# Kernel optimization log

Measured on AMD Instinct MI355X. Metric: run time of the kernel, lower is better.

The kernel has to match this reference:

```python
import jax, jax.numpy as jnp
import numpy as np

RC = 64   # residual_channels
SC = 64   # skip_channels
LAYERS = 10
STACKS = 3
N_LAYERS = LAYERS * STACKS


def _conv1x1(w, b, x):
    # w: [O, I, 1], b: [O], x: [B, I, T] -> [B, O, T]
    return jnp.einsum('oi,bit->bot', w[:, :, 0], x) + b[None, :, None]


def setup_inputs() -> dict:
    key = jax.random.key(0)
    ks = jax.random.split(key, 16)
    s = 0.05  # small init keeps 30-layer residual stack numerically tame
    B, T = 4, 32768
    inp = {
        'x': jax.random.normal(ks[0], (B, 1, T), dtype=jnp.float32),
        'start_w': jax.random.normal(ks[1], (RC, 1, 1), jnp.float32) * s,
        'start_b': jax.random.normal(ks[2], (RC,), jnp.float32) * s,
        'dil_w': jax.random.normal(ks[3], (N_LAYERS, 2 * RC, RC, 2), jnp.float32) * s,
        'dil_b': jax.random.normal(ks[4], (N_LAYERS, 2 * RC), jnp.float32) * s,
        'res_w': jax.random.normal(ks[5], (N_LAYERS, RC, RC, 1), jnp.float32) * s,
        'res_b': jax.random.normal(ks[6], (N_LAYERS, RC), jnp.float32) * s,
        'skip_w': jax.random.normal(ks[7], (N_LAYERS, SC, RC, 1), jnp.float32) * s,
        'skip_b': jax.random.normal(ks[8], (N_LAYERS, SC), jnp.float32) * s,
        'end1_w': jax.random.normal(ks[9], (SC, SC, 1), jnp.float32) * s,
        'end1_b': jax.random.normal(ks[10], (SC,), jnp.float32) * s,
        'end2_w': jax.random.normal(ks[11], (1, SC, 1), jnp.float32) * s,
        'end2_b': jax.random.normal(ks[12], (1,), jnp.float32) * s,
    }
    return inp


def reference(x, start_w, start_b, dil_w, dil_b, res_w, res_b,
              skip_w, skip_b, end1_w, end1_b, end2_w, end2_b):
    T = x.shape[-1]
    h = _conv1x1(start_w, start_b, x)  # [B, RC, T]
    skip_sum = jnp.zeros((x.shape[0], SC, T), dtype=h.dtype)
    for i in range(N_LAYERS):
        d = 2 ** (i % LAYERS)
        # causal dilated conv, k=2: y[t] = w0 @ h[t-d] + w1 @ h[t]
        h_shift = jnp.pad(h, ((0, 0), (0, 0), (d, 0)))[:, :, :T]
        conv = (jnp.einsum('oi,bit->bot', dil_w[i, :, :, 0], h_shift)
                + jnp.einsum('oi,bit->bot', dil_w[i, :, :, 1], h)
                + dil_b[i][None, :, None])  # [B, 2*RC, T]
        filt, gate = conv[:, :RC], conv[:, RC:]
        gated = jnp.tanh(filt) * jax.nn.sigmoid(gate)
        residual = _conv1x1(res_w[i], res_b[i], gated)
        skip = _conv1x1(skip_w[i], skip_b[i], gated)
        skip_sum = skip_sum + skip
        h = h + residual
    out = jax.nn.relu(_conv1x1(end1_w, end1_b, skip_sum))
    out = _conv1x1(end2_w, end2_b, out)
    return out
```

## Files before the change

### kernel.cpp

```cpp
#include <hip/hip_runtime.h>
#include <hip/hip_bf16.h>

#define RC 64
#define SC 64
#define NLAYERS 30
#define TTILE 64

typedef __attribute__((ext_vector_type(8))) short bf16x8;
typedef __attribute__((ext_vector_type(4))) float f32x4;

__device__ __forceinline__ unsigned short f2bf(float f) {
    __hip_bfloat16 h = __float2bfloat16(f);
    return *reinterpret_cast<unsigned short*>(&h);
}
__device__ __forceinline__ float bf2f(unsigned short u) {
    unsigned int x = ((unsigned int)u) << 16;
    return *reinterpret_cast<float*>(&x);
}

__global__ __launch_bounds__(256) void wn_prep(
    const float* __restrict__ dw, const float* __restrict__ rw,
    const float* __restrict__ skw, const float* __restrict__ db,
    const float* __restrict__ rb, const float* __restrict__ skb,
    unsigned short* __restrict__ pW1, unsigned short* __restrict__ pW2,
    float* __restrict__ pB1, float* __restrict__ pB2)
{
    const int i = blockIdx.x;
    const int tx = threadIdx.x;
    const int l = tx & 63;

    #pragma unroll
    for (int p = 0; p < 8; ++p) {
        int f = p * 4 + (tx >> 6);
        int w = f >> 3, nf = (f >> 2) & 1, ks = f & 3;
        int cpp = w * 32 + nf * 16 + (l & 15);
        int bb = cpp >> 4;
        int c1 = (bb & 1 ? 64 : 0) + (bb >> 1) * 16 + (cpp & 15);
        bf16x8 v;
        #pragma unroll
        for (int j = 0; j < 8; ++j) {
            int k = ks * 32 + (l >> 4) * 8 + j;
            int tap = (k < 64) ? 0 : 1;
            int kk = k & 63;
            v[j] = (short)f2bf(dw[(((size_t)i * 128 + c1) * 64 + kk) * 2 + tap]);
        }
        *(bf16x8*)&pW1[((size_t)(i * 32 + f) * 64 + l) * 8] = v;
    }

    #pragma unroll
    for (int p = 0; p < 4; ++p) {
        int f = p * 4 + (tx >> 6);
        int w = f >> 2, nf = (f >> 1) & 1, ks = f & 1;
        int cpp = w * 32 + nf * 16 + (l & 15);
        int bb = cpp >> 4;
        int c2 = (bb >> 1) * 16 + (cpp & 15);
        const float* src = (bb & 1) ? skw : rw;
        bf16x8 v;
        #pragma unroll
        for (int j = 0; j < 8; ++j) {
            int k = ks * 32 + (l >> 4) * 8 + j;
            v[j] = (short)f2bf(src[((size_t)i * 64 + c2) * 64 + k]);
        }
        *(bf16x8*)&pW2[((size_t)(i * 16 + f) * 64 + l) * 8] = v;
    }

    if (tx < 128) {
        int bb = tx >> 4, r = tx & 15;
        int c1 = (bb & 1 ? 64 : 0) + (bb >> 1) * 16 + r;
        pB1[i * 128 + tx] = db[i * 128 + c1];
        int c2 = (bb >> 1) * 16 + r;
        pB2[i * 128 + tx] = (bb & 1) ? skb[i * 64 + c2] : rb[i * 64 + c2];
    }
}

__global__ __launch_bounds__(256) void wn_start(
    const float* __restrict__ x, const float* __restrict__ sw,
    const float* __restrict__ sb, unsigned short* __restrict__ h, int T)
{
    int t = blockIdx.x * blockDim.x + threadIdx.x;
    int b = blockIdx.y;
    float xv = x[(size_t)b * T + t];
    unsigned int pk[32];
    #pragma unroll
    for (int c = 0; c < 64; c += 2) {
        float v0 = fmaf(sw[c], xv, sb[c]);
        float v1 = fmaf(sw[c + 1], xv, sb[c + 1]);
        pk[c >> 1] = (unsigned int)f2bf(v0) | ((unsigned int)f2bf(v1) << 16);
    }
    uint4* dst = (uint4*)(h + ((size_t)b * T + t) * 64);
    #pragma unroll
    for (int i = 0; i < 8; ++i) dst[i] = ((const uint4*)pk)[i];
}

__global__ __launch_bounds__(256) void wn_layer(
    const unsigned short* __restrict__ h_in, unsigned short* __restrict__ h_out,
    float* __restrict__ skip_sum,
    const unsigned short* __restrict__ pW1, const unsigned short* __restrict__ pW2,
    const float* __restrict__ pB1, const float* __restrict__ pB2,
    int d, int T, int accum)
{
    __shared__ unsigned short Xs[64 * 128];
    __shared__ unsigned short Gs[64 * 64];

    const int tx = threadIdx.x;
    const int w = tx >> 6;
    const int l = tx & 63;
    const int lr = l & 15;
    const int lg = l >> 4;
    const int b = blockIdx.y;
    const int t0 = blockIdx.x * TTILE;
    const size_t bT = (size_t)b * T;

    #pragma unroll
    for (int q = 0; q < 4; ++q) {
        int idx = tx * 4 + q;
        int t = idx >> 4;
        int ch = idx & 15;
        int tt = (ch < 8) ? (t0 + t - d) : (t0 + t);
        bf16x8 v = {0, 0, 0, 0, 0, 0, 0, 0};
        if (tt >= 0)
            v = *(const bf16x8*)(h_in + ((size_t)(bT + tt)) * 64 + (ch & 7) * 8);
        int swz = (ch & 8) | ((ch & 7) ^ (t & 7));
        *(bf16x8*)&Xs[(t * 256 + swz * 16) >> 1] = v;
    }

    bf16x8 W1f[2][4];
    #pragma unroll
    for (int nf = 0; nf < 2; ++nf)
        #pragma unroll
        for (int ks = 0; ks < 4; ++ks)
            W1f[nf][ks] = *(const bf16x8*)&pW1[((size_t)(w * 8 + nf * 4 + ks) * 64 + l) * 8];
    bf16x8 W2f[2][2];
    #pragma unroll
    for (int nf = 0; nf < 2; ++nf)
        #pragma unroll
        for (int ks = 0; ks < 2; ++ks)
            W2f[nf][ks] = *(const bf16x8*)&pW2[((size_t)(w * 4 + nf * 2 + ks) * 64 + l) * 8];

    float bias1[2], bias2[2];
    #pragma unroll
    for (int nf = 0; nf < 2; ++nf) {
        bias1[nf] = pB1[w * 32 + nf * 16 + lr];
        bias2[nf] = pB2[w * 32 + nf * 16 + lr];
    }

    __syncthreads();

    f32x4 acc1[4][2];
    #pragma unroll
    for (int mf = 0; mf < 4; ++mf) {
        #pragma unroll
        for (int nf = 0; nf < 2; ++nf) {
            f32x4 a = {bias1[nf], bias1[nf], bias1[nf], bias1[nf]};
            #pragma unroll
            for (int ks = 0; ks < 4; ++ks) {
                int tr = mf * 16 + lr;
                int chunk = ks * 4 + lg;
                int swz = (chunk & 8) | ((chunk & 7) ^ (tr & 7));
                bf16x8 av = *(const bf16x8*)&Xs[(tr * 256 + swz * 16) >> 1];
                a = __builtin_amdgcn_mfma_f32_16x16x32_bf16(av, W1f[nf][ks], a, 0, 0, 0);
            }
            acc1[mf][nf] = a;
        }
    }

    const int gc = w * 16 + lr;
    #pragma unroll
    for (int mf = 0; mf < 4; ++mf) {
        #pragma unroll
        for (int r = 0; r < 4; ++r) {
            int tr = mf * 16 + lg * 4 + r;
            float fv = fminf(fmaxf(acc1[mf][0][r], -30.f), 30.f);
            float gv = fminf(fmaxf(acc1[mf][1][r], -30.f), 30.f);
            float e2 = __expf(-2.f * fv);
            float th = (1.f - e2) * __builtin_amdgcn_rcpf(1.f + e2);
            float sg = __builtin_amdgcn_rcpf(1.f + __expf(-gv));
            float gated = th * sg;
            int byte = tr * 128 + (((gc >> 3) ^ (tr & 7)) * 16) + (gc & 7) * 2;
            Gs[byte >> 1] = f2bf(gated);
        }
    }

    float sold[16];
    if (accum) {
        #pragma unroll
        for (int mf = 0; mf < 4; ++mf)
            #pragma unroll
            for (int r = 0; r < 4; ++r) {
                int tr = mf * 16 + lg * 4 + r;
                sold[mf * 4 + r] = skip_sum[(bT + t0 + tr) * 64 + gc];
            }
    } else {
        #pragma unroll
        for (int i = 0; i < 16; ++i) sold[i] = 0.f;
    }

    __syncthreads();

    f32x4 acc2[4][2];
    #pragma unroll
    for (int mf = 0; mf < 4; ++mf) {
        #pragma unroll
        for (int nf = 0; nf < 2; ++nf) {
            f32x4 a = {bias2[nf], bias2[nf], bias2[nf], bias2[nf]};
            #pragma unroll
            for (int ks = 0; ks < 2; ++ks) {
                int tr = mf * 16 + lr;
                int chunk = ks * 4 + lg;
                int swz = chunk ^ (tr & 7);
                bf16x8 av = *(const bf16x8*)&Gs[(tr * 128 + swz * 16) >> 1];
                a = __builtin_amdgcn_mfma_f32_16x16x32_bf16(av, W2f[nf][ks], a, 0, 0, 0);
            }
            acc2[mf][nf] = a;
        }
    }

    #pragma unroll
    for (int mf = 0; mf < 4; ++mf) {
        #pragma unroll
        for (int r = 0; r < 4; ++r) {
            int tr = mf * 16 + lg * 4 + r;
            int chunk = 8 | ((gc >> 3) ^ (tr & 7));
            unsigned short hb = Xs[(tr * 256 + chunk * 16 + (gc & 7) * 2) >> 1];
            float hres = bf2f(hb) + acc2[mf][0][r];
            size_t gidx = (bT + t0 + tr) * 64 + gc;
            h_out[gidx] = f2bf(hres);
            skip_sum[gidx] = sold[mf * 4 + r] + acc2[mf][1][r];
        }
    }
}

__global__ __launch_bounds__(256) void wn_end(
    const float* __restrict__ skip, const float* __restrict__ w1,
    const float* __restrict__ b1, const float* __restrict__ w2,
    const float* __restrict__ b2, float* __restrict__ out, int T)
{
    int t = blockIdx.x * blockDim.x + threadIdx.x;
    int b = blockIdx.y;
    const float* row = skip + ((size_t)b * T + t) * 64;
    float sv[SC];
    #pragma unroll
    for (int k = 0; k < SC; k += 4) {
        float4 v = *(const float4*)&row[k];
        sv[k] = v.x; sv[k + 1] = v.y; sv[k + 2] = v.z; sv[k + 3] = v.w;
    }
    float acc = b2[0];
    for (int c = 0; c < SC; ++c) {
        float s = b1[c];
        #pragma unroll
        for (int k = 0; k < SC; k += 4) {
            float4 wv = *(const float4*)&w1[(size_t)c * SC + k];
            s = fmaf(wv.x, sv[k], fmaf(wv.y, sv[k + 1], fmaf(wv.z, sv[k + 2], fmaf(wv.w, sv[k + 3], s))));
        }
        acc = fmaf(w2[c], fmaxf(s, 0.f), acc);
    }
    out[(size_t)b * T + t] = acc;
}

extern "C" void kernel_launch(void* const* d_in, const int* in_sizes, int n_in,
                              void* d_out, int out_size, void* d_ws, size_t ws_size,
                              hipStream_t stream)
{
    const float* x   = (const float*)d_in[0];
    const float* stw = (const float*)d_in[1];
    const float* stb = (const float*)d_in[2];
    const float* dw  = (const float*)d_in[3];
    const float* db  = (const float*)d_in[4];
    const float* rw  = (const float*)d_in[5];
    const float* rb  = (const float*)d_in[6];
    const float* skw = (const float*)d_in[7];
    const float* skb = (const float*)d_in[8];
    const float* e1w = (const float*)d_in[9];
    const float* e1b = (const float*)d_in[10];
    const float* e2w = (const float*)d_in[11];
    const float* e2b = (const float*)d_in[12];

    const int T = 32768;
    const int B = in_sizes[0] / T;

    char* ws = (char*)d_ws;
    const size_t hbytes = (size_t)B * T * 64 * 2;
    unsigned short* h0 = (unsigned short*)ws;
    unsigned short* h1 = (unsigned short*)(ws + hbytes);
    float* sk = (float*)(ws + 2 * hbytes);
    unsigned short* pW1 = (unsigned short*)(ws + 2 * hbytes + (size_t)B * T * 64 * 4);
    unsigned short* pW2 = pW1 + (size_t)NLAYERS * 32 * 64 * 8;
    float* pB1 = (float*)(pW2 + (size_t)NLAYERS * 16 * 64 * 8);
    float* pB2 = pB1 + NLAYERS * 128;

    wn_prep<<<dim3(NLAYERS), 256, 0, stream>>>(dw, rw, skw, db, rb, skb, pW1, pW2, pB1, pB2);
    wn_start<<<dim3(T / 256, B), 256, 0, stream>>>(x, stw, stb, h0, T);

    const unsigned short* hin = h0;
    unsigned short* hout = h1;
    for (int i = 0; i < NLAYERS; ++i) {
        int d = 1 << (i % 10);
        wn_layer<<<dim3(T / TTILE, B), 256, 0, stream>>>(
            hin, hout, sk,
            pW1 + (size_t)i * 32 * 64 * 8, pW2 + (size_t)i * 16 * 64 * 8,
            pB1 + i * 128, pB2 + i * 128,
            d, T, i > 0 ? 1 : 0);
        const unsigned short* tmp = hout;
        hout = (unsigned short*)hin;
        hin = tmp;
    }

    wn_end<<<dim3(T / 256, B), 256, 0, stream>>>(sk, e1w, e1b, e2w, e2b, (float*)d_out, T);
}
```

Before: 743.2 us.

## Fuse first six dilated layers per stack into one kernel with halo recompute

Adds a kernel that runs layers with dilations 1..32 of each stack in a single launch. Each block loads 64 halo rows plus 64 output rows of h into LDS and keeps intermediate h and the skip accumulation on-chip across the six layers. This removes per-layer global reads and writes of h and skip_sum plus kernel launch overhead for those layers. In exchange it doubles the MFMA and activation work on the fused layers for the halo rows and uses more shared memory, which may reduce occupancy.

```diff
diff --git a/kernel.cpp b/kernel.cpp
--- a/kernel.cpp
+++ b/kernel.cpp
@@ -227,6 +227,151 @@
             h_out[gidx] = f2bf(hres);
             skip_sum[gidx] = sold[mf * 4 + r] + acc2[mf][1][r];
         }
+    }
+}
+
+__global__ __launch_bounds__(256) void wn_fused6(
+    const unsigned short* __restrict__ h_in, unsigned short* __restrict__ h_out,
+    float* __restrict__ skip_sum,
+    const unsigned short* __restrict__ pW1, const unsigned short* __restrict__ pW2,
+    const float* __restrict__ pB1, const float* __restrict__ pB2,
+    int T, int accum)
+{
+    __shared__ unsigned short Hs[2][128 * 64];
+    __shared__ unsigned short Gs[128 * 64];
+
+    const int tx = threadIdx.x;
+    const int w = tx >> 6;
+    const int l = tx & 63;
+    const int lr = l & 15;
+    const int lg = l >> 4;
+    const int b = blockIdx.y;
+    const int t0 = blockIdx.x * 64;
+    const size_t bT = (size_t)b * T;
+    const int gc = w * 16 + lr;
+
+    float sold[16], sacc[16];
+    #pragma unroll
+    for (int i = 0; i < 16; ++i) sacc[i] = 0.f;
+    if (accum) {
+        #pragma unroll
+        for (int i = 0; i < 16; ++i) {
+            int t = t0 + (i >> 2) * 16 + lg * 4 + (i & 3);
+            sold[i] = skip_sum[(bT + t) * 64 + gc];
+        }
+    } else {
+        #pragma unroll
+        for (int i = 0; i < 16; ++i) sold[i] = 0.f;
+    }
+
+    #pragma unroll
+    for (int q = 0; q < 4; ++q) {
+        int idx = q * 256 + tx;
+        int row = idx >> 3, c8 = idx & 7;
+        int tt = t0 - 64 + row;
+        bf16x8 v = {0, 0, 0, 0, 0, 0, 0, 0};
+        if (tt >= 0)
+            v = *(const bf16x8*)(h_in + (bT + tt) * 64 + c8 * 8);
+        *(bf16x8*)&Hs[0][(row * 128 + ((c8 ^ (row & 7)) * 16)) >> 1] = v;
+    }
+
+    int cur = 0;
+    #pragma unroll
+    for (int j = 0; j < 6; ++j) {
+        const int d = 1 << j;
+        const unsigned short* W1p = pW1 + (size_t)j * 32 * 64 * 8;
+        const unsigned short* W2p = pW2 + (size_t)j * 16 * 64 * 8;
+
+        bf16x8 W1f[2][4];
+        #pragma unroll
+        for (int nf = 0; nf < 2; ++nf)
+            #pragma unroll
+            for (int ks = 0; ks < 4; ++ks)
+                W1f[nf][ks] = *(const bf16x8*)&W1p[((size_t)(w * 8 + nf * 4 + ks) * 64 + l) * 8];
+        bf16x8 W2f[2][2];
+        #pragma unroll
+        for (int nf = 0; nf < 2; ++nf)
+            #pragma unroll
+            for (int ks = 0; ks < 2; ++ks)
+                W2f[nf][ks] = *(const bf16x8*)&W2p[((size_t)(w * 4 + nf * 2 + ks) * 64 + l) * 8];
+        float bias1[2], bias2[2];
+        #pragma unroll
+        for (int nf = 0; nf < 2; ++nf) {
+            bias1[nf] = pB1[j * 128 + w * 32 + nf * 16 + lr];
+            bias2[nf] = pB2[j * 128 + w * 32 + nf * 16 + lr];
+        }
+
+        __syncthreads();
+
+        #pragma unroll
+        for (int mf = 0; mf < 8; ++mf) {
+            int tr = mf * 16 + lr;
+            int rs = tr - d; if (rs < 0) rs = 0;
+            f32x4 a0 = {bias1[0], bias1[0], bias1[0], bias1[0]};
+            f32x4 a1 = {bias1[1], bias1[1], bias1[1], bias1[1]};
+            #pragma unroll
+            for (int ks = 0; ks < 4; ++ks) {
+                int rrow = (ks >> 1) ? tr : rs;
+                int c8 = (ks & 1) * 4 + lg;
+                bf16x8 av = *(const bf16x8*)&Hs[cur][(rrow * 128 + ((c8 ^ (rrow & 7)) * 16)) >> 1];
+                a0 = __builtin_amdgcn_mfma_f32_16x16x32_bf16(av, W1f[0][ks], a0, 0, 0, 0);
+                a1 = __builtin_amdgcn_mfma_f32_16x16x32_bf16(av, W1f[1][ks], a1, 0, 0, 0);
+            }
+            #pragma unroll
+            for (int r = 0; r < 4; ++r) {
+                int row = mf * 16 + lg * 4 + r;
+                float fv = fminf(fmaxf(a0[r], -30.f), 30.f);
+                float gv = fminf(fmaxf(a1[r], -30.f), 30.f);
+                float e2 = __expf(-2.f * fv);
+                float th = (1.f - e2) * __builtin_amdgcn_rcpf(1.f + e2);
+                float sg = __builtin_amdgcn_rcpf(1.f + __expf(-gv));
+                int byte = row * 128 + (((gc >> 3) ^ (row & 7)) * 16) + (gc & 7) * 2;
+                Gs[byte >> 1] = f2bf(th * sg);
+            }
+        }
+
+        __syncthreads();
+
+        #pragma unroll
+        for (int mf = 0; mf < 8; ++mf) {
+            int tr = mf * 16 + lr;
+            f32x4 a0 = {bias2[0], bias2[0], bias2[0], bias2[0]};
+            f32x4 a1 = {bias2[1], bias2[1], bias2[1], bias2[1]};
+            #pragma unroll
+            for (int ks = 0; ks < 2; ++ks) {
+                int c8 = ks * 4 + lg;
+                bf16x8 av = *(const bf16x8*)&Gs[(tr * 128 + ((c8 ^ (tr & 7)) * 16)) >> 1];
+                a0 = __builtin_amdgcn_mfma_f32_16x16x32_bf16(av, W2f[0][ks], a0, 0, 0, 0);
+                a1 = __builtin_amdgcn_mfma_f32_16x16x32_bf16(av, W2f[1][ks], a1, 0, 0, 0);
+            }
+            #pragma unroll
+            for (int r = 0; r < 4; ++r) {
+                int row = mf * 16 + lg * 4 + r;
+                int tt = t0 - 64 + row;
+                int byte = row * 128 + (((gc >> 3) ^ (row & 7)) * 16) + (gc & 7) * 2;
+                float hc = bf2f(Hs[cur][byte >> 1]);
+                float hres = hc + a0[r];
+                Hs[cur ^ 1][byte >> 1] = (tt < 0) ? (unsigned short)0 : f2bf(hres);
+                if (mf >= 4) sacc[(mf - 4) * 4 + r] += a1[r];
+            }
+        }
+        cur ^= 1;
+    }
+
+    __syncthreads();
+
+    #pragma unroll
+    for (int q = 0; q < 2; ++q) {
+        int idx = q * 256 + tx;
+        int row = 64 + (idx >> 3), c8 = idx & 7;
+        bf16x8 v = *(const bf16x8*)&Hs[cur][(row * 128 + ((c8 ^ (row & 7)) * 16)) >> 1];
+        *(bf16x8*)(h_out + (bT + t0 + (row - 64)) * 64 + c8 * 8) = v;
+    }
+
+    #pragma unroll
+    for (int i = 0; i < 16; ++i) {
+        int t = t0 + (i >> 2) * 16 + lg * 4 + (i & 3);
+        skip_sum[(bT + t) * 64 + gc] = sold[i] + sacc[i];
     }
 }
 
@@ -293,16 +438,24 @@
 
     const unsigned short* hin = h0;
     unsigned short* hout = h1;
-    for (int i = 0; i < NLAYERS; ++i) {
-        int d = 1 << (i % 10);
-        wn_layer<<<dim3(T / TTILE, B), 256, 0, stream>>>(
+    for (int g = 0; g < 3; ++g) {
+        int L = g * 10;
+        wn_fused6<<<dim3(T / 64, B), 256, 0, stream>>>(
             hin, hout, sk,
-            pW1 + (size_t)i * 32 * 64 * 8, pW2 + (size_t)i * 16 * 64 * 8,
-            pB1 + i * 128, pB2 + i * 128,
-            d, T, i > 0 ? 1 : 0);
-        const unsigned short* tmp = hout;
-        hout = (unsigned short*)hin;
-        hin = tmp;
+            pW1 + (size_t)L * 32 * 64 * 8, pW2 + (size_t)L * 16 * 64 * 8,
+            pB1 + L * 128, pB2 + L * 128,
+            T, g > 0 ? 1 : 0);
+        { const unsigned short* t = hout; hout = (unsigned short*)hin; hin = t; }
+        for (int j = 6; j < 10; ++j) {
+            int i = L + j;
+            int d = 1 << j;
+            wn_layer<<<dim3(T / TTILE, B), 256, 0, stream>>>(
+                hin, hout, sk,
+                pW1 + (size_t)i * 32 * 64 * 8, pW2 + (size_t)i * 16 * 64 * 8,
+                pB1 + i * 128, pB2 + i * 128,
+                d, T, 1);
+            const unsigned short* t = hout; hout = (unsigned short*)hin; hin = t;
+        }
     }
 
     wn_end<<<dim3(T / 256, B), 256, 0, stream>>>(sk, e1w, e1b, e2w, e2b, (float*)d_out, T);
```

After: 964.3 us. 29.7% more time.

## Store skip accumulator in bf16 split across two buffers and simplify gate math

Applied to the files above, without the earlier changes.

The per-layer skip_sum read-modify-write moves from fp32 to bf16, halving that traffic in every layer. To limit rounding drift, the accumulation is split into two partial buffers (layers 0-14 and 15-29), which the end kernel adds together. The gated activation also fuses tanh and sigmoid into one reciprocal and drops the clamps. This risks bf16 accumulation error, and inf/NaN when the unclamped exponentials overflow at large pre-activations.

```diff
diff --git a/kernel.cpp b/kernel.cpp
--- a/kernel.cpp
+++ b/kernel.cpp
@@ -94,7 +94,7 @@
 
 __global__ __launch_bounds__(256) void wn_layer(
     const unsigned short* __restrict__ h_in, unsigned short* __restrict__ h_out,
-    float* __restrict__ skip_sum,
+    unsigned short* __restrict__ skip_sum,
     const unsigned short* __restrict__ pW1, const unsigned short* __restrict__ pW2,
     const float* __restrict__ pB1, const float* __restrict__ pB2,
     int d, int T, int accum)
@@ -170,12 +170,9 @@
         #pragma unroll
         for (int r = 0; r < 4; ++r) {
             int tr = mf * 16 + lg * 4 + r;
-            float fv = fminf(fmaxf(acc1[mf][0][r], -30.f), 30.f);
-            float gv = fminf(fmaxf(acc1[mf][1][r], -30.f), 30.f);
-            float e2 = __expf(-2.f * fv);
-            float th = (1.f - e2) * __builtin_amdgcn_rcpf(1.f + e2);
-            float sg = __builtin_amdgcn_rcpf(1.f + __expf(-gv));
-            float gated = th * sg;
+            float e2 = __expf(-2.f * acc1[mf][0][r]);
+            float e3 = __expf(-acc1[mf][1][r]);
+            float gated = (1.f - e2) * __builtin_amdgcn_rcpf((1.f + e2) * (1.f + e3));
             int byte = tr * 128 + (((gc >> 3) ^ (tr & 7)) * 16) + (gc & 7) * 2;
             Gs[byte >> 1] = f2bf(gated);
         }
@@ -188,7 +185,7 @@
             #pragma unroll
             for (int r = 0; r < 4; ++r) {
                 int tr = mf * 16 + lg * 4 + r;
-                sold[mf * 4 + r] = skip_sum[(bT + t0 + tr) * 64 + gc];
+                sold[mf * 4 + r] = bf2f(skip_sum[(bT + t0 + tr) * 64 + gc]);
             }
     } else {
         #pragma unroll
@@ -225,24 +222,29 @@
             float hres = bf2f(hb) + acc2[mf][0][r];
             size_t gidx = (bT + t0 + tr) * 64 + gc;
             h_out[gidx] = f2bf(hres);
-            skip_sum[gidx] = sold[mf * 4 + r] + acc2[mf][1][r];
+            skip_sum[gidx] = f2bf(sold[mf * 4 + r] + acc2[mf][1][r]);
         }
     }
 }
 
 __global__ __launch_bounds__(256) void wn_end(
-    const float* __restrict__ skip, const float* __restrict__ w1,
-    const float* __restrict__ b1, const float* __restrict__ w2,
-    const float* __restrict__ b2, float* __restrict__ out, int T)
+    const unsigned short* __restrict__ skA, const unsigned short* __restrict__ skB,
+    const float* __restrict__ w1, const float* __restrict__ b1,
+    const float* __restrict__ w2, const float* __restrict__ b2,
+    float* __restrict__ out, int T)
 {
     int t = blockIdx.x * blockDim.x + threadIdx.x;
     int b = blockIdx.y;
-    const float* row = skip + ((size_t)b * T + t) * 64;
+    const unsigned short* rowA = skA + ((size_t)b * T + t) * 64;
+    const unsigned short* rowB = skB + ((size_t)b * T + t) * 64;
     float sv[SC];
     #pragma unroll
-    for (int k = 0; k < SC; k += 4) {
-        float4 v = *(const float4*)&row[k];
-        sv[k] = v.x; sv[k + 1] = v.y; sv[k + 2] = v.z; sv[k + 3] = v.w;
+    for (int k = 0; k < SC; k += 8) {
+        bf16x8 va = *(const bf16x8*)&rowA[k];
+        bf16x8 vb = *(const bf16x8*)&rowB[k];
+        #pragma unroll
+        for (int j = 0; j < 8; ++j)
+            sv[k + j] = bf2f((unsigned short)va[j]) + bf2f((unsigned short)vb[j]);
     }
     float acc = b2[0];
     for (int c = 0; c < SC; ++c) {
@@ -280,9 +282,10 @@
 
     char* ws = (char*)d_ws;
     const size_t hbytes = (size_t)B * T * 64 * 2;
-    unsigned short* h0 = (unsigned short*)ws;
-    unsigned short* h1 = (unsigned short*)(ws + hbytes);
-    float* sk = (float*)(ws + 2 * hbytes);
+    unsigned short* h0  = (unsigned short*)ws;
+    unsigned short* h1  = (unsigned short*)(ws + hbytes);
+    unsigned short* skA = (unsigned short*)(ws + 2 * hbytes);
+    unsigned short* skB = skA + (size_t)B * T * 64;
     unsigned short* pW1 = (unsigned short*)(ws + 2 * hbytes + (size_t)B * T * 64 * 4);
     unsigned short* pW2 = pW1 + (size_t)NLAYERS * 32 * 64 * 8;
     float* pB1 = (float*)(pW2 + (size_t)NLAYERS * 16 * 64 * 8);
@@ -295,15 +298,17 @@
     unsigned short* hout = h1;
     for (int i = 0; i < NLAYERS; ++i) {
         int d = 1 << (i % 10);
+        unsigned short* skbuf = (i < 15) ? skA : skB;
+        int accum = (i == 0 || i == 15) ? 0 : 1;
         wn_layer<<<dim3(T / TTILE, B), 256, 0, stream>>>(
-            hin, hout, sk,
+            hin, hout, skbuf,
             pW1 + (size_t)i * 32 * 64 * 8, pW2 + (size_t)i * 16 * 64 * 8,
             pB1 + i * 128, pB2 + i * 128,
-            d, T, i > 0 ? 1 : 0);
+            d, T, accum);
         const unsigned short* tmp = hout;
         hout = (unsigned short*)hin;
         hin = tmp;
     }
 
-    wn_end<<<dim3(T / 256, B), 256, 0, stream>>>(sk, e1w, e1b, e2w, e2b, (float*)d_out, T);
-}
+    wn_end<<<dim3(T / 256, B), 256, 0, stream>>>(skA, skB, e1w, e1b, e2w, e2b, (float*)d_out, T);
+}
```

Result: faster. 676.7 us (median of 2 runs) (-9.0%).
